# Performance work log

Hardware: AMD Instinct MI355X
Metric: run time of the kernel (lower is better)

The kernel has to match this reference:

```python
import jax, jax.numpy as jnp
import numpy as np

B = 64          # batch
C = 80          # num_classes
IN_CH = 300     # word-embedding channel
J = 8192        # JOINT_EMB_SIZE (linear_intermediate)
S = 8           # pooling_stride
OUT = J // S    # out_in_tmp = 1024


def setup_inputs() -> dict:
    key = jax.random.key(0)
    ks = jax.random.split(key, 8)
    w = lambda k, sh: jax.random.normal(k, sh, jnp.float32) * 0.02
    return {
        "feature": jax.random.normal(ks[0], (B, 2048, 14, 14), jnp.float32),
        "inp": jax.random.normal(ks[1], (1, C, IN_CH), jnp.float32),
        "A": jax.random.uniform(ks[2], (C, C), jnp.float32),  # positive co-occurrence adjacency
        "W_gc1": w(ks[3], (IN_CH, 1024)),
        "W_gc2": w(ks[4], (1024, 2048)),
        "W_img": w(ks[5], (J, 2048)),
        "b_img": jnp.zeros((J,), jnp.float32),
        "W_cls": w(ks[6], (J, 2048)),
        "b_cls": jnp.zeros((J,), jnp.float32),
        "W_ml": w(ks[7], (C, C * OUT)),
        "b_ml": jnp.zeros((C,), jnp.float32),
    }


def reference(feature, inp, A, W_gc1, W_gc2, W_img, b_img, W_cls, b_cls, W_ml, b_ml):
    # backbone output -> MaxPool2d(14,14) over a 14x14 map == global spatial max
    feat = feature.max(axis=(2, 3))                       # [B, 2048]

    # gen_adj(A).detach(): D = diag(rowsum(A)^-0.5); adj = D @ A.T @ D
    dinv = jnp.sum(A, axis=1) ** -0.5                     # [C]
    adj = jax.lax.stop_gradient(A.T * dinv[:, None] * dinv[None, :])  # [C, C]

    # two GCN layers on label embeddings
    x = adj @ (inp[0] @ W_gc1)                            # [C, 1024]
    x = jax.nn.leaky_relu(x, 0.2)
    x = adj @ (x @ W_gc2)                                 # [C, 2048]

    # MFB bilinear fusion (vectorized form of the nested batch/class loops;
    # dropout is identity in eval mode)
    img = feat @ W_img.T + b_img                          # [B, J]
    cls = x @ W_cls.T + b_cls                             # [C, J]
    # sum-pool over the stride axis of the elementwise product:
    # iq[b,c,o] = sum_s img[b,o*S+s] * cls[c,o*S+s]
    pooled = jnp.einsum('bos,cos->bco',
                        img.reshape(B, OUT, S),
                        cls.reshape(C, OUT, S))           # [B, C, OUT]
    # torch.cat order over class columns -> c-major flatten, then ML_fc_layer
    out = pooled.reshape(B, C * OUT) @ W_ml.T + b_ml      # [B, C]
    return out
```

## Files before the change

### kernel.cpp

```cpp
#include <hip/hip_runtime.h>
#include <hip/hip_bf16.h>
#include <cstdint>
#include <cstddef>

typedef float  f32x4  __attribute__((ext_vector_type(4)));
typedef __bf16 bf16x8 __attribute__((ext_vector_type(8)));
typedef unsigned short u16x8 __attribute__((ext_vector_type(8)));

__device__ __forceinline__ unsigned short f2bf(float f) {
    unsigned u = __float_as_uint(f);
    u += 0x7FFFu + ((u >> 16) & 1u);
    return (unsigned short)(u >> 16);
}


constexpr size_t OFF_FEATB = 0;
constexpr size_t OFF_X2B   = 262144;
constexpr size_t OFF_XB    = 425984;
constexpr size_t OFF_IMG   = 753664;
constexpr size_t OFF_CLS   = 2850816;
constexpr size_t OFF_G     = 5472256;


__device__ __forceinline__ void maxpool_role(int vbid, const float* __restrict__ feature,
                                             unsigned short* __restrict__ featb,
                                             float4* tile ) {
    int t = threadIdx.x;
    const float4* src = (const float4*)(feature + (size_t)vbid * 32 * 196);
    #pragma unroll
    for (int pass = 0; pass < 6; ++pass)
        tile[pass * 256 + t] = src[pass * 256 + t];
    if (t < 32) tile[1536 + t] = src[1536 + t];
    __syncthreads();

    int r = t >> 3, q = t & 7;
    const float4* row = tile + r * 49;
    float4 v0 = row[q],      v1 = row[q + 8],  v2 = row[q + 16];
    float4 v3 = row[q + 24], v4 = row[q + 32], v5 = row[q + 40];
    float m0 = fmaxf(fmaxf(v0.x, v0.y), fmaxf(v0.z, v0.w));
    float m1 = fmaxf(fmaxf(v1.x, v1.y), fmaxf(v1.z, v1.w));
    float m2 = fmaxf(fmaxf(v2.x, v2.y), fmaxf(v2.z, v2.w));
    float m3 = fmaxf(fmaxf(v3.x, v3.y), fmaxf(v3.z, v3.w));
    float m4 = fmaxf(fmaxf(v4.x, v4.y), fmaxf(v4.z, v4.w));
    float m5 = fmaxf(fmaxf(v5.x, v5.y), fmaxf(v5.z, v5.w));
    float m = fmaxf(fmaxf(fmaxf(m0, m1), fmaxf(m2, m3)), fmaxf(m4, m5));
    if (q == 0) {
        float4 d = row[48];
        m = fmaxf(m, fmaxf(fmaxf(d.x, d.y), fmaxf(d.z, d.w)));
    }
    #pragma unroll
    for (int off = 1; off < 8; off <<= 1) m = fmaxf(m, __shfl_xor(m, off));
    if (q == 0) featb[vbid * 32 + r] = f2bf(m);
}

__device__ __forceinline__ void gcn_front_role(int idx, const float* __restrict__ inp,
                                               const float* __restrict__ W1,
                                               const float* __restrict__ A,
                                               unsigned short* __restrict__ x2b,
                                               float* smem) {
    float* dinv = smem;
    float* ys   = smem + 80;
    float* xs   = smem + 720;
    int t = threadIdx.x;
    int j = t & 7, slot = t >> 3;
    int j0 = idx * 8;
    int c0 = slot, c1 = slot + 32, c2 = slot + 64;
    bool has3 = (slot < 16);

    if (t < 80) {
        const float4* ar = (const float4*)(A + t * 80);
        float4 s4 = {0.f, 0.f, 0.f, 0.f};
        #pragma unroll
        for (int q = 0; q < 20; q++) {
            float4 v = ar[q];
            s4.x += v.x; s4.y += v.y; s4.z += v.z; s4.w += v.w;
        }
        dinv[t] = 1.0f / sqrtf(s4.x + s4.y + s4.z + s4.w);
    }

    const float* wcol = W1 + j0 + j;
    const float* i0 = inp + c0 * 300;
    const float* i1 = inp + c1 * 300;
    const float* i2 = inp + c2 * 300;
    float a0 = 0.f, a1 = 0.f, a2 = 0.f;
    for (int k = 0; k < 300; k += 4) {
        float w[4], p0[4], p1[4], p2[4];
        #pragma unroll
        for (int u = 0; u < 4; u++) w[u] = wcol[(size_t)(k + u) * 1024];
        #pragma unroll
        for (int u = 0; u < 4; u++) p0[u] = i0[k + u];
        #pragma unroll
        for (int u = 0; u < 4; u++) p1[u] = i1[k + u];
        if (has3) {
            #pragma unroll
            for (int u = 0; u < 4; u++) p2[u] = i2[k + u];
        }
        #pragma unroll
        for (int u = 0; u < 4; u++) {
            a0 = fmaf(p0[u], w[u], a0);
            a1 = fmaf(p1[u], w[u], a1);
            if (has3) a2 = fmaf(p2[u], w[u], a2);
        }
    }
    __syncthreads();
    ys[c0 * 8 + j] = dinv[c0] * a0;
    ys[c1 * 8 + j] = dinv[c1] * a1;
    if (has3) ys[c2 * 8 + j] = dinv[c2] * a2;
    __syncthreads();

    float b0 = 0.f, b1 = 0.f, b2 = 0.f;
    #pragma unroll 4
    for (int e = 0; e < 80; e++) {
        float y = ys[e * 8 + j];
        b0 = fmaf(A[e * 80 + c0], y, b0);
        b1 = fmaf(A[e * 80 + c1], y, b1);
        if (has3) b2 = fmaf(A[e * 80 + c2], y, b2);
    }
    b0 *= dinv[c0];
    b1 *= dinv[c1];
    b2 *= has3 ? dinv[c2] : 0.f;
    if (b0 < 0.f) b0 *= 0.2f;
    if (b1 < 0.f) b1 *= 0.2f;
    if (b2 < 0.f) b2 *= 0.2f;
    __syncthreads();
    xs[c0 * 8 + j] = dinv[c0] * b0;
    xs[c1 * 8 + j] = dinv[c1] * b1;
    if (has3) xs[c2 * 8 + j] = dinv[c2] * b2;
    __syncthreads();

    float d0 = 0.f, d1 = 0.f, d2 = 0.f;
    #pragma unroll 4
    for (int e = 0; e < 80; e++) {
        float x = xs[e * 8 + j];
        d0 = fmaf(A[e * 80 + c0], x, d0);
        d1 = fmaf(A[e * 80 + c1], x, d1);
        if (has3) d2 = fmaf(A[e * 80 + c2], x, d2);
    }
    x2b[c0 * 1024 + j0 + j] = f2bf(d0 * dinv[c0]);
    x2b[c1 * 1024 + j0 + j] = f2bf(d1 * dinv[c1]);
    if (has3) x2b[c2 * 1024 + j0 + j] = f2bf(d2 * dinv[c2]);
}

template <int MF>
__device__ __forceinline__ void gemm_block(int bx, const unsigned short* __restrict__ X,
                                           const float* __restrict__ W,
                                           const float* __restrict__ bias,
                                           float* __restrict__ outf,
                                           unsigned short* __restrict__ outb,
                                           int N, int K, float (*red)[64][21]) {
    int tid = threadIdx.x;
    int ks = tid >> 6, lane = tid & 63;
    int n = bx * 16 + (lane & 15);
    int rowa = lane & 15;
    int koff = (lane >> 4) * 8;
    int Kc = K >> 2;
    int k0 = ks * Kc;

    f32x4 acc[MF];
    #pragma unroll
    for (int i = 0; i < MF; i++) acc[i] = (f32x4)(0.f);

    const float* wrow = W + (size_t)n * K;

    #pragma unroll 2
    for (int k = k0; k < k0 + Kc; k += 32) {
        float4 w0 = *(const float4*)(wrow + k + koff);
        float4 w1 = *(const float4*)(wrow + k + koff + 4);
        u16x8 bu;
        bu[0] = f2bf(w0.x); bu[1] = f2bf(w0.y); bu[2] = f2bf(w0.z); bu[3] = f2bf(w0.w);
        bu[4] = f2bf(w1.x); bu[5] = f2bf(w1.y); bu[6] = f2bf(w1.z); bu[7] = f2bf(w1.w);
        bf16x8 bf = __builtin_bit_cast(bf16x8, bu);
        #pragma unroll
        for (int mf = 0; mf < MF; mf++) {
            u16x8 au = *(const u16x8*)(X + (size_t)(mf * 16 + rowa) * K + k + koff);
            acc[mf] = __builtin_amdgcn_mfma_f32_16x16x32_bf16(
                __builtin_bit_cast(bf16x8, au), bf, acc[mf], 0, 0, 0);
        }
    }

    #pragma unroll
    for (int mf = 0; mf < MF; mf++)
        #pragma unroll
        for (int i = 0; i < 4; i++)
            red[ks][lane][mf * 4 + i] = acc[mf][i];
    __syncthreads();

    int lane2 = tid & 63, sg = tid >> 6;
    int n2 = bx * 16 + (lane2 & 15);
    float b = bias ? bias[n2] : 0.f;
    #pragma unroll
    for (int mf = 0; mf < MF; mf++) {
        int slot = mf * 4 + sg;
        float s = red[0][lane2][slot] + red[1][lane2][slot]
                + red[2][lane2][slot] + red[3][lane2][slot] + b;
        int row = mf * 16 + (lane2 >> 4) * 4 + sg;
        size_t o = (size_t)row * N + n2;
        if (outf) outf[o] = s;
        if (outb) outb[o] = f2bf(s);
    }
}

template <int MF>
__device__ __forceinline__ void gemm_block_kn(int bx, const unsigned short* __restrict__ X,
                                              const float* __restrict__ Wkn,
                                              const float* __restrict__ bias,
                                              float* __restrict__ outf,
                                              unsigned short* __restrict__ outb,
                                              int N, int K, float (*red)[64][21]) {
    int tid = threadIdx.x;
    int ks = tid >> 6, lane = tid & 63;
    int n = bx * 16 + (lane & 15);
    int rowa = lane & 15;
    int koff = (lane >> 4) * 8;
    int Kc = K >> 2;
    int k0 = ks * Kc;

    f32x4 acc[MF];
    #pragma unroll
    for (int i = 0; i < MF; i++) acc[i] = (f32x4)(0.f);

    #pragma unroll 2
    for (int k = k0; k < k0 + Kc; k += 32) {
        float w[8];
        #pragma unroll
        for (int i = 0; i < 8; i++) w[i] = Wkn[(size_t)(k + koff + i) * N + n];
        u16x8 bu;
        #pragma unroll
        for (int i = 0; i < 8; i++) bu[i] = f2bf(w[i]);
        bf16x8 bf = __builtin_bit_cast(bf16x8, bu);
        #pragma unroll
        for (int mf = 0; mf < MF; mf++) {
            u16x8 au = *(const u16x8*)(X + (size_t)(mf * 16 + rowa) * K + k + koff);
            acc[mf] = __builtin_amdgcn_mfma_f32_16x16x32_bf16(
                __builtin_bit_cast(bf16x8, au), bf, acc[mf], 0, 0, 0);
        }
    }

    #pragma unroll
    for (int mf = 0; mf < MF; mf++)
        #pragma unroll
        for (int i = 0; i < 4; i++)
            red[ks][lane][mf * 4 + i] = acc[mf][i];
    __syncthreads();

    int lane2 = tid & 63, sg = tid >> 6;
    int n2 = bx * 16 + (lane2 & 15);
    float b = bias ? bias[n2] : 0.f;
    #pragma unroll
    for (int mf = 0; mf < MF; mf++) {
        int slot = mf * 4 + sg;
        float s = red[0][lane2][slot] + red[1][lane2][slot]
                + red[2][lane2][slot] + red[3][lane2][slot] + b;
        int row = mf * 16 + (lane2 >> 4) * 4 + sg;
        size_t o = (size_t)row * N + n2;
        if (outf) outf[o] = s;
        if (outb) outb[o] = f2bf(s);
    }
}


__global__ __launch_bounds__(256, 4) void kD1(const float* __restrict__ feature,
                                              unsigned short* __restrict__ featb,
                                              const float* __restrict__ inp,
                                              const float* __restrict__ W1,
                                              const float* __restrict__ A,
                                              unsigned short* __restrict__ x2b) {
    __shared__ __align__(16) float smem[6272];
    int b = blockIdx.x;
    if (b < 128) gcn_front_role(b, inp, W1, A, x2b, smem);
    else         maxpool_role(b - 128, feature, featb, (float4*)smem);
}

__global__ __launch_bounds__(256, 4) void kD2(const unsigned short* __restrict__ featb,
                                              const float* __restrict__ W_img,
                                              const float* __restrict__ b_img,
                                              float* __restrict__ img,
                                              const unsigned short* __restrict__ x2b,
                                              const float* __restrict__ W_gc2,
                                              unsigned short* __restrict__ xb) {
    __shared__ __align__(16) float red[4][64][21];
    int b = blockIdx.x;
    if (b < 512) gemm_block<4>(b, featb, W_img, b_img, img, nullptr, 8192, 2048, red);
    else         gemm_block_kn<5>(b - 512, x2b, W_gc2, nullptr, nullptr, xb, 2048, 1024, red);
}

__global__ __launch_bounds__(256, 4) void kD3(const unsigned short* __restrict__ xb,
                                              const float* __restrict__ W_cls,
                                              const float* __restrict__ b_cls,
                                              float* __restrict__ cls) {
    __shared__ __align__(16) float red[4][64][21];
    gemm_block<5>(blockIdx.x, xb, W_cls, b_cls, cls, nullptr, 8192, 2048, red);
}

__global__ __launch_bounds__(256, 4) void kD4(const float* __restrict__ cls,
                                              const float* __restrict__ W_ml,
                                              float* __restrict__ G) {
    __shared__ __align__(16) float smem[8 * 80 * 16];
    float (*wml)[80][16] = (float (*)[80][16])smem;
    int idx = blockIdx.x;
    int o0  = (idx & 63) * 16;
    int c2b = (idx >> 6) * 8;
    int j0  = o0 * 8;
    for (int i = threadIdx.x; i < 8 * 80 * 16; i += 256) {
        int ol = i & 15, c = (i >> 4) % 80, c2 = i / 1280;
        wml[c2][c][ol] = W_ml[(size_t)(c2b + c2) * 81920 + c * 1024 + o0 + ol];
    }
    __syncthreads();
    int jl  = threadIdx.x & 127;
    int c2h = (threadIdx.x >> 7) * 4;
    int ol  = jl >> 3;
    float acc[4] = {0.f, 0.f, 0.f, 0.f};
    for (int c = 0; c < 80; c++) {
        float cv = cls[(size_t)c * 8192 + j0 + jl];
        #pragma unroll
        for (int i = 0; i < 4; i++) acc[i] = fmaf(cv, wml[c2h + i][c][ol], acc[i]);
    }
    #pragma unroll
    for (int i = 0; i < 4; i++) G[(size_t)(c2b + c2h + i) * 8192 + j0 + jl] = acc[i];
}

__global__ __launch_bounds__(256, 2) void kD5(const float* __restrict__ img,
                                              const float* __restrict__ G,
                                              const float* __restrict__ b_ml,
                                              float* __restrict__ out) {
    __shared__ float sm[4][8];
    int b = blockIdx.x / 10, cg = blockIdx.x % 10;
    int kc = threadIdx.x >> 6, lane = threadIdx.x & 63;
    const float* ib = img + (size_t)b * 8192 + kc * 2048;
    const float* gb = G + (size_t)(cg * 8) * 8192 + kc * 2048;
    float acc[8] = {0.f, 0.f, 0.f, 0.f, 0.f, 0.f, 0.f, 0.f};
    #pragma unroll
    for (int step = 0; step < 8; step++) {
        int k = step * 256 + lane * 4;
        float4 iv = *(const float4*)(ib + k);
        float4 gv[8];
        #pragma unroll
        for (int i = 0; i < 8; i++) gv[i] = *(const float4*)(gb + (size_t)i * 8192 + k);
        #pragma unroll
        for (int i = 0; i < 8; i++) {
            acc[i] = fmaf(iv.x, gv[i].x, acc[i]);
            acc[i] = fmaf(iv.y, gv[i].y, acc[i]);
            acc[i] = fmaf(iv.z, gv[i].z, acc[i]);
            acc[i] = fmaf(iv.w, gv[i].w, acc[i]);
        }
    }
    #pragma unroll
    for (int i = 0; i < 8; i++) {
        float v = acc[i];
        #pragma unroll
        for (int off = 32; off; off >>= 1) v += __shfl_xor(v, off);
        if (lane == 0) sm[kc][i] = v;
    }
    __syncthreads();
    if (threadIdx.x < 8) {
        int i = threadIdx.x;
        float s = b_ml[cg * 8 + i] + sm[0][i] + sm[1][i] + sm[2][i] + sm[3][i];
        out[(size_t)b * 80 + cg * 8 + i] = s;
    }
}

extern "C" void kernel_launch(void* const* d_in, const int* in_sizes, int n_in,
                              void* d_out, int out_size, void* d_ws, size_t ws_size,
                              hipStream_t stream) {
    (void)in_sizes; (void)n_in; (void)out_size; (void)ws_size;
    const float* feature = (const float*)d_in[0];
    const float* inp     = (const float*)d_in[1];
    const float* A       = (const float*)d_in[2];
    const float* W_gc1   = (const float*)d_in[3];
    const float* W_gc2   = (const float*)d_in[4];
    const float* W_img   = (const float*)d_in[5];
    const float* b_img   = (const float*)d_in[6];
    const float* W_cls   = (const float*)d_in[7];
    const float* b_cls   = (const float*)d_in[8];
    const float* W_ml    = (const float*)d_in[9];
    const float* b_ml    = (const float*)d_in[10];
    float* out = (float*)d_out;
    char*  ws  = (char*)d_ws;

    unsigned short* featb = (unsigned short*)(ws + OFF_FEATB);
    unsigned short* x2b   = (unsigned short*)(ws + OFF_X2B);
    unsigned short* xb    = (unsigned short*)(ws + OFF_XB);
    float* img  = (float*)(ws + OFF_IMG);
    float* cls  = (float*)(ws + OFF_CLS);
    float* G    = (float*)(ws + OFF_G);

    kD1<<<4224, 256, 0, stream>>>(feature, featb, inp, W_gc1, A, x2b);
    kD2<<<640,  256, 0, stream>>>(featb, W_img, b_img, img, x2b, W_gc2, xb);
    kD3<<<512,  256, 0, stream>>>(xb, W_cls, b_cls, cls);
    kD4<<<640,  256, 0, stream>>>(cls, W_ml, G);
    kD5<<<640,  256, 0, stream>>>(img, G, b_ml, out);
}
```

Measured before the change: 156.5 us.

## Split GCN front into a parallel inp@W1 stage and rebalance image GEMM across kernels

The first GCN layer's inp@W_gc1 product moves out of the 128-block front role into its own 320-block role. That role uses float4 weight loads and a 4-way K split reduced in shared memory, and writes y0 to a new workspace buffer. The adjacency and leaky-relu stage becomes a separate role in the next kernel. The W_img GEMM blocks are split across two kernels so they overlap the now-serialized GCN stages (x1/x2, then W_gc2). This adds one more launch and a global round trip for y0, in exchange for shortening the serial critical path of the GCN chain.

Result: faster. 132.3 us (-15.4%).

```diff
diff --git a/kernel.cpp b/kernel.cpp
--- a/kernel.cpp
+++ b/kernel.cpp
@@ -20,6 +20,7 @@
 constexpr size_t OFF_IMG   = 753664;
 constexpr size_t OFF_CLS   = 2850816;
 constexpr size_t OFF_G     = 5472256;
+constexpr size_t OFF_Y0    = 8093696;
 
 
 __device__ __forceinline__ void maxpool_role(int vbid, const float* __restrict__ feature,
@@ -53,11 +54,45 @@
     if (q == 0) featb[vbid * 32 + r] = f2bf(m);
 }
 
-__device__ __forceinline__ void gcn_front_role(int idx, const float* __restrict__ inp,
-                                               const float* __restrict__ W1,
-                                               const float* __restrict__ A,
-                                               unsigned short* __restrict__ x2b,
-                                               float* smem) {
+__device__ __forceinline__ void y0_role(int idx, const float* __restrict__ inp,
+                                        const float* __restrict__ W1,
+                                        float* __restrict__ y0g, float4* red) {
+    int c = idx >> 2;
+    int j = (idx & 3) * 256 + (threadIdx.x & 63) * 4;
+    int ks = threadIdx.x >> 6;
+    const float* ir = inp + c * 300 + ks * 75;
+    const float* wp = W1 + (size_t)(ks * 75) * 1024 + j;
+    float4 acc = {0.f, 0.f, 0.f, 0.f};
+    for (int k = 0; k < 75; k += 3) {
+        float a0 = ir[k], a1 = ir[k + 1], a2 = ir[k + 2];
+        float4 w0 = *(const float4*)(wp + (size_t)k * 1024);
+        float4 w1 = *(const float4*)(wp + (size_t)(k + 1) * 1024);
+        float4 w2 = *(const float4*)(wp + (size_t)(k + 2) * 1024);
+        acc.x = fmaf(a0, w0.x, acc.x); acc.y = fmaf(a0, w0.y, acc.y);
+        acc.z = fmaf(a0, w0.z, acc.z); acc.w = fmaf(a0, w0.w, acc.w);
+        acc.x = fmaf(a1, w1.x, acc.x); acc.y = fmaf(a1, w1.y, acc.y);
+        acc.z = fmaf(a1, w1.z, acc.z); acc.w = fmaf(a1, w1.w, acc.w);
+        acc.x = fmaf(a2, w2.x, acc.x); acc.y = fmaf(a2, w2.y, acc.y);
+        acc.z = fmaf(a2, w2.z, acc.z); acc.w = fmaf(a2, w2.w, acc.w);
+    }
+    int jq = threadIdx.x & 63;
+    red[ks * 64 + jq] = __builtin_bit_cast(float4, acc);
+    __syncthreads();
+    if (ks == 0) {
+        float4 s0 = red[jq], s1 = red[64 + jq], s2 = red[128 + jq], s3 = red[192 + jq];
+        float4 s;
+        s.x = s0.x + s1.x + s2.x + s3.x;
+        s.y = s0.y + s1.y + s2.y + s3.y;
+        s.z = s0.z + s1.z + s2.z + s3.z;
+        s.w = s0.w + s1.w + s2.w + s3.w;
+        *(float4*)(y0g + (size_t)c * 1024 + j) = s;
+    }
+}
+
+__device__ __forceinline__ void x1x2_role(int idx, const float* __restrict__ y0g,
+                                          const float* __restrict__ A,
+                                          unsigned short* __restrict__ x2b,
+                                          float* smem) {
     float* dinv = smem;
     float* ys   = smem + 80;
     float* xs   = smem + 720;
@@ -77,35 +112,10 @@
         }
         dinv[t] = 1.0f / sqrtf(s4.x + s4.y + s4.z + s4.w);
     }
-
-    const float* wcol = W1 + j0 + j;
-    const float* i0 = inp + c0 * 300;
-    const float* i1 = inp + c1 * 300;
-    const float* i2 = inp + c2 * 300;
-    float a0 = 0.f, a1 = 0.f, a2 = 0.f;
-    for (int k = 0; k < 300; k += 4) {
-        float w[4], p0[4], p1[4], p2[4];
-        #pragma unroll
-        for (int u = 0; u < 4; u++) w[u] = wcol[(size_t)(k + u) * 1024];
-        #pragma unroll
-        for (int u = 0; u < 4; u++) p0[u] = i0[k + u];
-        #pragma unroll
-        for (int u = 0; u < 4; u++) p1[u] = i1[k + u];
-        if (has3) {
-            #pragma unroll
-            for (int u = 0; u < 4; u++) p2[u] = i2[k + u];
-        }
-        #pragma unroll
-        for (int u = 0; u < 4; u++) {
-            a0 = fmaf(p0[u], w[u], a0);
-            a1 = fmaf(p1[u], w[u], a1);
-            if (has3) a2 = fmaf(p2[u], w[u], a2);
-        }
-    }
-    __syncthreads();
-    ys[c0 * 8 + j] = dinv[c0] * a0;
-    ys[c1 * 8 + j] = dinv[c1] * a1;
-    if (has3) ys[c2 * 8 + j] = dinv[c2] * a2;
+    __syncthreads();
+    ys[c0 * 8 + j] = dinv[c0] * y0g[(size_t)c0 * 1024 + j0 + j];
+    ys[c1 * 8 + j] = dinv[c1] * y0g[(size_t)c1 * 1024 + j0 + j];
+    if (has3) ys[c2 * 8 + j] = dinv[c2] * y0g[(size_t)c2 * 1024 + j0 + j];
     __syncthreads();
 
     float b0 = 0.f, b1 = 0.f, b2 = 0.f;
@@ -259,42 +269,54 @@
 }
 
 
-__global__ __launch_bounds__(256, 4) void kD1(const float* __restrict__ feature,
-                                              unsigned short* __restrict__ featb,
-                                              const float* __restrict__ inp,
-                                              const float* __restrict__ W1,
-                                              const float* __restrict__ A,
-                                              unsigned short* __restrict__ x2b) {
+__global__ __launch_bounds__(256, 4) void kA(const float* __restrict__ feature,
+                                             unsigned short* __restrict__ featb,
+                                             const float* __restrict__ inp,
+                                             const float* __restrict__ W1,
+                                             float* __restrict__ y0g) {
     __shared__ __align__(16) float smem[6272];
     int b = blockIdx.x;
-    if (b < 128) gcn_front_role(b, inp, W1, A, x2b, smem);
-    else         maxpool_role(b - 128, feature, featb, (float4*)smem);
-}
-
-__global__ __launch_bounds__(256, 4) void kD2(const unsigned short* __restrict__ featb,
-                                              const float* __restrict__ W_img,
-                                              const float* __restrict__ b_img,
-                                              float* __restrict__ img,
-                                              const unsigned short* __restrict__ x2b,
-                                              const float* __restrict__ W_gc2,
-                                              unsigned short* __restrict__ xb) {
+    if (b < 320) y0_role(b, inp, W1, y0g, (float4*)smem);
+    else         maxpool_role(b - 320, feature, featb, (float4*)smem);
+}
+
+__global__ __launch_bounds__(256, 4) void kB(const float* __restrict__ y0g,
+                                             const float* __restrict__ A,
+                                             unsigned short* __restrict__ x2b,
+                                             const unsigned short* __restrict__ featb,
+                                             const float* __restrict__ W_img,
+                                             const float* __restrict__ b_img,
+                                             float* __restrict__ img) {
     __shared__ __align__(16) float red[4][64][21];
     int b = blockIdx.x;
-    if (b < 512) gemm_block<4>(b, featb, W_img, b_img, img, nullptr, 8192, 2048, red);
-    else         gemm_block_kn<5>(b - 512, x2b, W_gc2, nullptr, nullptr, xb, 2048, 1024, red);
-}
-
-__global__ __launch_bounds__(256, 4) void kD3(const unsigned short* __restrict__ xb,
-                                              const float* __restrict__ W_cls,
-                                              const float* __restrict__ b_cls,
-                                              float* __restrict__ cls) {
+    if (b < 128) x1x2_role(b, y0g, A, x2b, (float*)red);
+    else         gemm_block<4>(b - 128, featb, W_img, b_img, img, nullptr, 8192, 2048, red);
+}
+
+__global__ __launch_bounds__(256, 4) void kC(const unsigned short* __restrict__ x2b,
+                                             const float* __restrict__ W_gc2,
+                                             unsigned short* __restrict__ xb,
+                                             const unsigned short* __restrict__ featb,
+                                             const float* __restrict__ W_img,
+                                             const float* __restrict__ b_img,
+                                             float* __restrict__ img) {
+    __shared__ __align__(16) float red[4][64][21];
+    int b = blockIdx.x;
+    if (b < 128) gemm_block_kn<5>(b, x2b, W_gc2, nullptr, nullptr, xb, 2048, 1024, red);
+    else         gemm_block<4>(b - 128 + 384, featb, W_img, b_img, img, nullptr, 8192, 2048, red);
+}
+
+__global__ __launch_bounds__(256, 4) void kD(const unsigned short* __restrict__ xb,
+                                             const float* __restrict__ W_cls,
+                                             const float* __restrict__ b_cls,
+                                             float* __restrict__ cls) {
     __shared__ __align__(16) float red[4][64][21];
     gemm_block<5>(blockIdx.x, xb, W_cls, b_cls, cls, nullptr, 8192, 2048, red);
 }
 
-__global__ __launch_bounds__(256, 4) void kD4(const float* __restrict__ cls,
-                                              const float* __restrict__ W_ml,
-                                              float* __restrict__ G) {
+__global__ __launch_bounds__(256, 4) void kE(const float* __restrict__ cls,
+                                             const float* __restrict__ W_ml,
+                                             float* __restrict__ G) {
     __shared__ __align__(16) float smem[8 * 80 * 16];
     float (*wml)[80][16] = (float (*)[80][16])smem;
     int idx = blockIdx.x;
@@ -319,10 +341,10 @@
     for (int i = 0; i < 4; i++) G[(size_t)(c2b + c2h + i) * 8192 + j0 + jl] = acc[i];
 }
 
-__global__ __launch_bounds__(256, 2) void kD5(const float* __restrict__ img,
-                                              const float* __restrict__ G,
-                                              const float* __restrict__ b_ml,
-                                              float* __restrict__ out) {
+__global__ __launch_bounds__(256, 2) void kF(const float* __restrict__ img,
+                                             const float* __restrict__ G,
+                                             const float* __restrict__ b_ml,
+                                             float* __restrict__ out) {
     __shared__ float sm[4][8];
     int b = blockIdx.x / 10, cg = blockIdx.x % 10;
     int kc = threadIdx.x >> 6, lane = threadIdx.x & 63;
@@ -383,10 +405,12 @@
     float* img  = (float*)(ws + OFF_IMG);
     float* cls  = (float*)(ws + OFF_CLS);
     float* G    = (float*)(ws + OFF_G);
-
-    kD1<<<4224, 256, 0, stream>>>(feature, featb, inp, W_gc1, A, x2b);
-    kD2<<<640,  256, 0, stream>>>(featb, W_img, b_img, img, x2b, W_gc2, xb);
-    kD3<<<512,  256, 0, stream>>>(xb, W_cls, b_cls, cls);
-    kD4<<<640,  256, 0, stream>>>(cls, W_ml, G);
-    kD5<<<640,  256, 0, stream>>>(img, G, b_ml, out);
-}
+    float* y0g  = (float*)(ws + OFF_Y0);
+
+    kA<<<4416, 256, 0, stream>>>(feature, featb, inp, W_gc1, y0g);
+    kB<<<512,  256, 0, stream>>>(y0g, A, x2b, featb, W_img, b_img, img);
+    kC<<<256,  256, 0, stream>>>(x2b, W_gc2, xb, featb, W_img, b_img, img);
+    kD<<<512,  256, 0, stream>>>(xb, W_cls, b_cls, cls);
+    kE<<<640,  256, 0, stream>>>(cls, W_ml, G);
+    kF<<<640,  256, 0, stream>>>(img, G, b_ml, out);
+}
```

## Stage GCN front weights and inputs in LDS with wider column tiles

Applied to the files above, without the earlier changes.

The first GCN layer now copies a 16-column slice of W_gc1 into shared memory in transposed form, streams the label embeddings through LDS in chunks of 16 classes, and computes the dot products with float4 LDS reads. This replaces the strided global loads that happened per thread. Each block covers 16 columns instead of 8, so there are half as many GCN blocks. The kernel's shared memory grows to about 49KB and its occupancy hint drops from 4 to 2, which also applies to the maxpool blocks that share the kernel and may slow that memory-bound part.

Result: no change. 157.7 us (+0.8%).

```diff
diff --git a/kernel.cpp b/kernel.cpp
--- a/kernel.cpp
+++ b/kernel.cpp
@@ -58,14 +58,14 @@
                                                const float* __restrict__ A,
                                                unsigned short* __restrict__ x2b,
                                                float* smem) {
-    float* dinv = smem;
-    float* ys   = smem + 80;
-    float* xs   = smem + 720;
+    float* W1sT = smem;
+    float* inpS = smem + 4864;
+    float* y0s  = smem + 9728;
+    float* x1s  = smem + 11008;
+    float* dinv = smem + 12288;
     int t = threadIdx.x;
-    int j = t & 7, slot = t >> 3;
-    int j0 = idx * 8;
-    int c0 = slot, c1 = slot + 32, c2 = slot + 64;
-    bool has3 = (slot < 16);
+    int jj = t & 15, cg = t >> 4;
+    int j0 = idx * 16;
 
     if (t < 80) {
         const float4* ar = (const float4*)(A + t * 80);
@@ -77,68 +77,62 @@
         }
         dinv[t] = 1.0f / sqrtf(s4.x + s4.y + s4.z + s4.w);
     }
-
-    const float* wcol = W1 + j0 + j;
-    const float* i0 = inp + c0 * 300;
-    const float* i1 = inp + c1 * 300;
-    const float* i2 = inp + c2 * 300;
-    float a0 = 0.f, a1 = 0.f, a2 = 0.f;
-    for (int k = 0; k < 300; k += 4) {
-        float w[4], p0[4], p1[4], p2[4];
-        #pragma unroll
-        for (int u = 0; u < 4; u++) w[u] = wcol[(size_t)(k + u) * 1024];
-        #pragma unroll
-        for (int u = 0; u < 4; u++) p0[u] = i0[k + u];
-        #pragma unroll
-        for (int u = 0; u < 4; u++) p1[u] = i1[k + u];
-        if (has3) {
-            #pragma unroll
-            for (int u = 0; u < 4; u++) p2[u] = i2[k + u];
-        }
-        #pragma unroll
-        for (int u = 0; u < 4; u++) {
-            a0 = fmaf(p0[u], w[u], a0);
-            a1 = fmaf(p1[u], w[u], a1);
-            if (has3) a2 = fmaf(p2[u], w[u], a2);
-        }
-    }
-    __syncthreads();
-    ys[c0 * 8 + j] = dinv[c0] * a0;
-    ys[c1 * 8 + j] = dinv[c1] * a1;
-    if (has3) ys[c2 * 8 + j] = dinv[c2] * a2;
-    __syncthreads();
-
-    float b0 = 0.f, b1 = 0.f, b2 = 0.f;
-    #pragma unroll 4
-    for (int e = 0; e < 80; e++) {
-        float y = ys[e * 8 + j];
-        b0 = fmaf(A[e * 80 + c0], y, b0);
-        b1 = fmaf(A[e * 80 + c1], y, b1);
-        if (has3) b2 = fmaf(A[e * 80 + c2], y, b2);
-    }
-    b0 *= dinv[c0];
-    b1 *= dinv[c1];
-    b2 *= has3 ? dinv[c2] : 0.f;
-    if (b0 < 0.f) b0 *= 0.2f;
-    if (b1 < 0.f) b1 *= 0.2f;
-    if (b2 < 0.f) b2 *= 0.2f;
-    __syncthreads();
-    xs[c0 * 8 + j] = dinv[c0] * b0;
-    xs[c1 * 8 + j] = dinv[c1] * b1;
-    if (has3) xs[c2 * 8 + j] = dinv[c2] * b2;
-    __syncthreads();
-
-    float d0 = 0.f, d1 = 0.f, d2 = 0.f;
-    #pragma unroll 4
-    for (int e = 0; e < 80; e++) {
-        float x = xs[e * 8 + j];
-        d0 = fmaf(A[e * 80 + c0], x, d0);
-        d1 = fmaf(A[e * 80 + c1], x, d1);
-        if (has3) d2 = fmaf(A[e * 80 + c2], x, d2);
-    }
-    x2b[c0 * 1024 + j0 + j] = f2bf(d0 * dinv[c0]);
-    x2b[c1 * 1024 + j0 + j] = f2bf(d1 * dinv[c1]);
-    if (has3) x2b[c2 * 1024 + j0 + j] = f2bf(d2 * dinv[c2]);
+    for (int i = t; i < 300 * 16; i += 256) {
+        int k = i >> 4, j = i & 15;
+        W1sT[j * 304 + k] = W1[(size_t)k * 1024 + j0 + j];
+    }
+
+    for (int ch = 0; ch < 5; ++ch) {
+        __syncthreads();
+        for (int i = t; i < 16 * 300; i += 256) {
+            int c = i / 300, k = i - c * 300;
+            inpS[c * 304 + k] = inp[(size_t)(ch * 16 + c) * 300 + k];
+        }
+        __syncthreads();
+        const float4* ip4 = (const float4*)(inpS + cg * 304);
+        const float4* wp4 = (const float4*)(W1sT + jj * 304);
+        float4 a = {0.f, 0.f, 0.f, 0.f};
+        #pragma unroll 5
+        for (int k4 = 0; k4 < 75; ++k4) {
+            float4 iv = ip4[k4], wv = wp4[k4];
+            a.x = fmaf(iv.x, wv.x, a.x);
+            a.y = fmaf(iv.y, wv.y, a.y);
+            a.z = fmaf(iv.z, wv.z, a.z);
+            a.w = fmaf(iv.w, wv.w, a.w);
+        }
+        y0s[(ch * 16 + cg) * 16 + jj] = (a.x + a.y) + (a.z + a.w);
+    }
+    __syncthreads();
+
+    #pragma unroll
+    for (int rep = 0; rep < 5; ++rep) {
+        int c = rep * 16 + cg;
+        y0s[c * 16 + jj] *= dinv[c];
+    }
+    __syncthreads();
+
+    #pragma unroll
+    for (int rep = 0; rep < 5; ++rep) {
+        int c = rep * 16 + cg;
+        float b = 0.f;
+        #pragma unroll 4
+        for (int e = 0; e < 80; e++)
+            b = fmaf(A[e * 80 + c], y0s[e * 16 + jj], b);
+        b *= dinv[c];
+        if (b < 0.f) b *= 0.2f;
+        x1s[c * 16 + jj] = dinv[c] * b;
+    }
+    __syncthreads();
+
+    #pragma unroll
+    for (int rep = 0; rep < 5; ++rep) {
+        int c = rep * 16 + cg;
+        float d = 0.f;
+        #pragma unroll 4
+        for (int e = 0; e < 80; e++)
+            d = fmaf(A[e * 80 + c], x1s[e * 16 + jj], d);
+        x2b[c * 1024 + j0 + jj] = f2bf(d * dinv[c]);
+    }
 }
 
 template <int MF>
@@ -259,42 +253,42 @@
 }
 
 
-__global__ __launch_bounds__(256, 4) void kD1(const float* __restrict__ feature,
-                                              unsigned short* __restrict__ featb,
-                                              const float* __restrict__ inp,
-                                              const float* __restrict__ W1,
-                                              const float* __restrict__ A,
-                                              unsigned short* __restrict__ x2b) {
-    __shared__ __align__(16) float smem[6272];
+__global__ __launch_bounds__(256, 2) void kA(const float* __restrict__ feature,
+                                             unsigned short* __restrict__ featb,
+                                             const float* __restrict__ inp,
+                                             const float* __restrict__ W1,
+                                             const float* __restrict__ A,
+                                             unsigned short* __restrict__ x2b) {
+    __shared__ __align__(16) float smem[12368];
     int b = blockIdx.x;
-    if (b < 128) gcn_front_role(b, inp, W1, A, x2b, smem);
-    else         maxpool_role(b - 128, feature, featb, (float4*)smem);
-}
-
-__global__ __launch_bounds__(256, 4) void kD2(const unsigned short* __restrict__ featb,
-                                              const float* __restrict__ W_img,
-                                              const float* __restrict__ b_img,
-                                              float* __restrict__ img,
-                                              const unsigned short* __restrict__ x2b,
-                                              const float* __restrict__ W_gc2,
-                                              unsigned short* __restrict__ xb) {
+    if (b < 64) gcn_front_role(b, inp, W1, A, x2b, smem);
+    else        maxpool_role(b - 64, feature, featb, (float4*)smem);
+}
+
+__global__ __launch_bounds__(256, 4) void kB(const unsigned short* __restrict__ featb,
+                                             const float* __restrict__ W_img,
+                                             const float* __restrict__ b_img,
+                                             float* __restrict__ img,
+                                             const unsigned short* __restrict__ x2b,
+                                             const float* __restrict__ W_gc2,
+                                             unsigned short* __restrict__ xb) {
     __shared__ __align__(16) float red[4][64][21];
     int b = blockIdx.x;
     if (b < 512) gemm_block<4>(b, featb, W_img, b_img, img, nullptr, 8192, 2048, red);
     else         gemm_block_kn<5>(b - 512, x2b, W_gc2, nullptr, nullptr, xb, 2048, 1024, red);
 }
 
-__global__ __launch_bounds__(256, 4) void kD3(const unsigned short* __restrict__ xb,
-                                              const float* __restrict__ W_cls,
-                                              const float* __restrict__ b_cls,
-                                              float* __restrict__ cls) {
+__global__ __launch_bounds__(256, 4) void kC(const unsigned short* __restrict__ xb,
+                                             const float* __restrict__ W_cls,
+                                             const float* __restrict__ b_cls,
+                                             float* __restrict__ cls) {
     __shared__ __align__(16) float red[4][64][21];
     gemm_block<5>(blockIdx.x, xb, W_cls, b_cls, cls, nullptr, 8192, 2048, red);
 }
 
-__global__ __launch_bounds__(256, 4) void kD4(const float* __restrict__ cls,
-                                              const float* __restrict__ W_ml,
-                                              float* __restrict__ G) {
+__global__ __launch_bounds__(256, 4) void kD(const float* __restrict__ cls,
+                                             const float* __restrict__ W_ml,
+                                             float* __restrict__ G) {
     __shared__ __align__(16) float smem[8 * 80 * 16];
     float (*wml)[80][16] = (float (*)[80][16])smem;
     int idx = blockIdx.x;
@@ -319,10 +313,10 @@
     for (int i = 0; i < 4; i++) G[(size_t)(c2b + c2h + i) * 8192 + j0 + jl] = acc[i];
 }
 
-__global__ __launch_bounds__(256, 2) void kD5(const float* __restrict__ img,
-                                              const float* __restrict__ G,
-                                              const float* __restrict__ b_ml,
-                                              float* __restrict__ out) {
+__global__ __launch_bounds__(256, 2) void kE(const float* __restrict__ img,
+                                             const float* __restrict__ G,
+                                             const float* __restrict__ b_ml,
+                                             float* __restrict__ out) {
     __shared__ float sm[4][8];
     int b = blockIdx.x / 10, cg = blockIdx.x % 10;
     int kc = threadIdx.x >> 6, lane = threadIdx.x & 63;
@@ -384,9 +378,9 @@
     float* cls  = (float*)(ws + OFF_CLS);
     float* G    = (float*)(ws + OFF_G);
 
-    kD1<<<4224, 256, 0, stream>>>(feature, featb, inp, W_gc1, A, x2b);
-    kD2<<<640,  256, 0, stream>>>(featb, W_img, b_img, img, x2b, W_gc2, xb);
-    kD3<<<512,  256, 0, stream>>>(xb, W_cls, b_cls, cls);
-    kD4<<<640,  256, 0, stream>>>(cls, W_ml, G);
-    kD5<<<640,  256, 0, stream>>>(img, G, b_ml, out);
-}
+    kA<<<4160, 256, 0, stream>>>(feature, featb, inp, W_gc1, A, x2b);
+    kB<<<640,  256, 0, stream>>>(featb, W_img, b_img, img, x2b, W_gc2, xb);
+    kC<<<512,  256, 0, stream>>>(xb, W_cls, b_cls, cls);
+    kD<<<640,  256, 0, stream>>>(cls, W_ml, G);
+    kE<<<640,  256, 0, stream>>>(img, G, b_ml, out);
+}
```
